# Kernel tuning notes

Hardware: AMD Instinct MI355X
Metric: run time of the kernel (lower is better)

## Reference

```python
import math
import jax, jax.numpy as jnp
import numpy as np

B, N, D, NC, TMAX = 8, 4096, 1024, 512, 1000


def setup_inputs() -> dict:
    key = jax.random.key(0)
    ks = jax.random.split(key, 12)
    tokens = jax.random.normal(ks[0], (B, N, D), jnp.float32)
    ctx_C = jax.random.normal(ks[1], (B, NC, D), jnp.float32)
    t = jax.random.randint(ks[2], (B,), 0, TMAX, dtype=jnp.int32)
    rare_mask = jax.random.bernoulli(ks[3], 0.05, (B, N))
    # Linear params stored as (in, out); scaled so scores straddle 0.5
    ctx_w = jax.random.normal(ks[4], (D, D // 4), jnp.float32) / math.sqrt(D)
    ctx_b = jax.random.normal(ks[5], (D // 4,), jnp.float32) * 0.01
    t_proj_w = jax.random.normal(ks[6], (D, D), jnp.float32) / math.sqrt(D)
    t_proj_b = jax.random.normal(ks[7], (D,), jnp.float32) * 0.01
    HIN = D + D // 4 + D  # 2304
    w1 = jax.random.normal(ks[8], (HIN, D // 2), jnp.float32) / math.sqrt(HIN)
    b1 = jax.random.normal(ks[9], (D // 2,), jnp.float32) * 0.01
    w2 = jax.random.normal(ks[10], (D // 2,), jnp.float32) * 0.1
    b2 = jnp.zeros((1,), jnp.float32)
    return {"tokens": tokens, "ctx_C": ctx_C, "t": t, "rare_mask": rare_mask,
            "ctx_w": ctx_w, "ctx_b": ctx_b, "t_proj_w": t_proj_w,
            "t_proj_b": t_proj_b, "w1": w1, "b1": b1, "w2": w2, "b2": b2}


def reference(tokens, ctx_C, t, rare_mask, ctx_w, ctx_b, t_proj_w, t_proj_b, w1, b1, w2, b2):
    Bb, Nn, Dd = tokens.shape
    half = Dd // 2
    # sinusoidal timestep embedding buffer (matches torch register_buffer)
    freq = jnp.exp(-math.log(10000.0) * jnp.arange(half, dtype=jnp.float32) / max(half - 1, 1))
    # bottlenecked context: mean over ctx tokens -> (B, D//4)
    ctx_bn = ctx_C.mean(axis=1) @ ctx_w + ctx_b
    args = t.astype(jnp.float32)[:, None] * freq[None, :]            # (B, half)
    emb = jnp.concatenate([jnp.sin(args), jnp.cos(args)], axis=-1)   # (B, D)
    t_emb = emb @ t_proj_w + t_proj_b                                # (B, D)
    x = jnp.concatenate([
        tokens,
        jnp.broadcast_to(ctx_bn[:, None, :], (Bb, Nn, Dd // 4)),
        jnp.broadcast_to(t_emb[:, None, :], (Bb, Nn, Dd)),
    ], axis=-1)                                                       # (B, N, 2.25D)
    h = jax.nn.relu(x @ w1 + b1)                                      # (B, N, D//2)
    scores = jax.nn.sigmoid(h @ w2 + b2)                              # (B, N)
    skip = (scores > 0.5) & jnp.logical_not(rare_mask)
    min_active = max(1, int(Nn * 0.2))
    active = jnp.logical_not(skip).sum(axis=-1)                       # (B,)
    deficit = jnp.maximum(min_active - active, 0)                     # (B,)
    masked = jnp.where(skip, scores, jnp.inf)
    rank = jnp.argsort(jnp.argsort(masked, axis=-1), axis=-1)         # rank among skipped, ascending score
    skip = skip & jnp.logical_not(rank < deficit[:, None])
    return skip, scores
```

## Files before the change

### kernel.cpp

```cpp
#include <hip/hip_runtime.h>
#include <math.h>

#define NN 4096
#define DD 1024
#define M_TOT 32768
#define H1 512
#define MIN_ACTIVE 819
#define MARGIN 0.03f
#define MAXFIX 8192

typedef __bf16 bf16x8 __attribute__((ext_vector_type(8)));
typedef float f32x4 __attribute__((ext_vector_type(4)));

__device__ __forceinline__ unsigned short f2bf(float f) {
    unsigned int u = __float_as_uint(f);
    return (unsigned short)((u + 0x7FFFu + ((u >> 16) & 1u)) >> 16);
}

__device__ __forceinline__ void glds16(const unsigned short* g, unsigned short* l) {
    __builtin_amdgcn_global_load_lds(
        (const __attribute__((address_space(1))) unsigned int*)g,
        (__attribute__((address_space(3))) unsigned int*)l, 16, 0, 0);
}

__global__ void convB_kernel(const float* __restrict__ w1, unsigned short* __restrict__ w1tt,
                             const unsigned char* __restrict__ rare, int* __restrict__ mode,
                             int* __restrict__ fixcnt) {
    __shared__ float tile[32][65];
    __shared__ int nonbin, oneoff;
    int t = blockIdx.x;
    int c0 = blockIdx.y * 64;
    int tid = threadIdx.x;
    #pragma unroll
    for (int i = 0; i < 8; ++i) {
        int idx = tid + 256 * i;
        int kk = idx >> 6, cc = idx & 63;
        tile[kk][cc] = w1[(size_t)(t * 32 + kk) * H1 + c0 + cc];
    }
    __syncthreads();
    {
        int cc = tid >> 2, jp = tid & 3;
        int c = c0 + cc;
        int j = jp ^ ((c >> 1) & 3);
        unsigned int w[4];
        #pragma unroll
        for (int q = 0; q < 4; ++q)
            w[q] = (unsigned int)f2bf(tile[j * 8 + 2 * q][cc])
                 | ((unsigned int)f2bf(tile[j * 8 + 2 * q + 1][cc]) << 16);
        uint4 v; v.x = w[0]; v.y = w[1]; v.z = w[2]; v.w = w[3];
        *(uint4*)(w1tt + ((size_t)t * 512 + c) * 32 + jp * 8) = v;
    }
    if (blockIdx.x == 0 && blockIdx.y == 0) {
        if (tid == 0) { nonbin = 0; oneoff = 0; *fixcnt = 0; }
        __syncthreads();
        int lnon = 0, lone = 0;
        for (int i = tid; i < 32768; i += 256) {
            unsigned char b = rare[i];
            if (b > 1) lnon = 1;
            else if (b == 1 && (i & 3) != 0) lone = 1;
        }
        if (lnon) atomicOr(&nonbin, 1);
        if (lone) atomicOr(&oneoff, 1);
        __syncthreads();
        if (tid == 0) *mode = nonbin ? 2 : (oneoff ? 1 : 0);
    }
}

__global__ void pmean_kernel(const float* __restrict__ ctx, float* __restrict__ pmean) {
    int blk = blockIdx.x;
    int b = blk >> 5, dq = (blk >> 3) & 3, nz = blk & 7;
    int d = dq * 256 + threadIdx.x;
    const float* base = ctx + ((size_t)(b * 512 + nz * 64)) * DD + d;
    float acc = 0.f;
    for (int n = 0; n < 64; ++n) acc += base[(size_t)n * DD];
    pmean[(b * 8 + nz) * DD + d] = acc;
}

__global__ void prep_kernel(const float* __restrict__ pmean, const int* __restrict__ t,
                            float* __restrict__ mean, float* __restrict__ embf) {
    int idx = blockIdx.x * 256 + threadIdx.x;
    int b = idx >> 10, j = idx & 1023;
    float s = 0.f;
    for (int nz = 0; nz < 8; ++nz) s += pmean[(b * 8 + nz) * DD + j];
    mean[idx] = s * (1.f / 512.f);
    int jj = j & 511;
    double arg = (double)t[b] * exp((-log(10000.0) / 511.0) * (double)jj);
    embf[idx] = (float)((j < 512) ? sin(arg) : cos(arg));
}

__global__ __launch_bounds__(256) void midk_kernel(
    const float* __restrict__ mean, const float* __restrict__ embf,
    const float* __restrict__ ctx_w, const float* __restrict__ ctx_b,
    const float* __restrict__ tpw, const float* __restrict__ tpb,
    float* __restrict__ ctx_bn, float* __restrict__ t_emb) {
    __shared__ float red8[8][32];
    __shared__ float red4[4][64];
    int tid = threadIdx.x;
    if (blockIdx.x < 64) {
        int b = blockIdx.x >> 3, cg = blockIdx.x & 7;
        int c = cg * 32 + (tid & 31), ks = tid >> 5;
        const float* mb = mean + b * DD + ks * 128;
        const float* wb = ctx_w + (size_t)(ks * 128) * 256 + c;
        float acc = 0.f;
        for (int i = 0; i < 128; ++i) acc += mb[i] * wb[(size_t)i * 256];
        red8[ks][tid & 31] = acc;
        __syncthreads();
        if (tid < 32) {
            float s = 0.f;
            for (int k = 0; k < 8; ++k) s += red8[k][tid];
            ctx_bn[b * 256 + cg * 32 + tid] = s + ctx_b[cg * 32 + tid];
        }
    } else {
        int blk = blockIdx.x - 64;
        int b = blk >> 4, cg = blk & 15;
        int c = cg * 64 + (tid & 63), ks = tid >> 6;
        const float* eb = embf + b * DD + ks * 256;
        const float* wb = tpw + (size_t)(ks * 256) * DD + c;
        float acc = 0.f;
        for (int i = 0; i < 256; ++i) acc += eb[i] * wb[(size_t)i * DD];
        red4[ks][tid & 63] = acc;
        __syncthreads();
        if (tid < 64) {
            float s = red4[0][tid] + red4[1][tid] + red4[2][tid] + red4[3][tid];
            t_emb[b * DD + cg * 64 + tid] = s + tpb[cg * 64 + tid];
        }
    }
}

__global__ void baseh_kernel(const float* __restrict__ ctx_bn, const float* __restrict__ t_emb,
                             const float* __restrict__ w1, const float* __restrict__ b1,
                             float* __restrict__ base_h) {
    __shared__ float red[8][32];
    int b = blockIdx.x, cg = blockIdx.y;
    int c = cg * 32 + (threadIdx.x & 31), ks = threadIdx.x >> 5;
    float acc = 0.f;
    for (int i = 0; i < 160; ++i) {
        int k = ks * 160 + i;
        float v = (k < 256) ? ctx_bn[b * 256 + k] : t_emb[b * DD + k - 256];
        acc += v * w1[(size_t)(1024 + k) * H1 + c];
    }
    red[ks][threadIdx.x & 31] = acc;
    __syncthreads();
    if (threadIdx.x < 32) {
        float s = 0.f;
        for (int k = 0; k < 8; ++k) s += red[k][threadIdx.x];
        base_h[b * H1 + cg * 32 + threadIdx.x] = s + b1[cg * 32 + threadIdx.x];
    }
}

__global__ __launch_bounds__(512, 4) void gemm_kernel(
    const float* __restrict__ tokens, const unsigned short* __restrict__ w1tt,
    const float* __restrict__ baseh, const float* __restrict__ w2,
    float* __restrict__ part) {
    __shared__ unsigned short As[128 * 40];
    __shared__ unsigned short Bs[2][256 * 32];
    __shared__ float red[128][4];
    int tid = threadIdx.x;
    int lane = tid & 63, wid = tid >> 6;
    int wm = wid >> 2, wn = wid & 3;
    int la = lane & 15, lk = lane >> 4;
    int row0 = blockIdx.x * 128;
    int half = blockIdx.y;
    const unsigned short* wsrc = w1tt + (size_t)half * 256 * 32;

    f32x4 acc[4][4];
    #pragma unroll
    for (int i = 0; i < 4; ++i)
        #pragma unroll
        for (int j = 0; j < 4; ++j)
            acc[i][j] = (f32x4){0.f, 0.f, 0.f, 0.f};

    float4 sa[2];
    #define LOAD_A(kt_) { \
        _Pragma("unroll") \
        for (int i = 0; i < 2; ++i) { \
            int id = tid + 512 * i; \
            int r = id >> 3, xk = id & 7; \
            sa[i] = *(const float4*)(tokens + (size_t)(row0 + r) * DD + (kt_) + xk * 4); \
        } }
    #define WRITE_A() { \
        _Pragma("unroll") \
        for (int i = 0; i < 2; ++i) { \
            int id = tid + 512 * i; \
            int r = id >> 3, xk = id & 7; \
            ushort4 h; \
            h.x = f2bf(sa[i].x); h.y = f2bf(sa[i].y); \
            h.z = f2bf(sa[i].z); h.w = f2bf(sa[i].w); \
            *(ushort4*)(As + r * 40 + xk * 4) = h; \
        } }
    #define STAGE_B(t_, bb_) { \
        const unsigned short* gsrc = wsrc + (size_t)(t_) * 512 * 32; \
        _Pragma("unroll") \
        for (int q = 0; q < 2; ++q) { \
            int chunk = wid * 2 + q; \
            glds16(gsrc + chunk * 512 + lane * 8, &Bs[bb_][chunk * 512]); \
        } }

    STAGE_B(0, 0);
    LOAD_A(0);
    WRITE_A();
    __syncthreads();

    for (int t = 0; t < 32; ++t) {
        int bb = t & 1;
        if (t < 31) {
            STAGE_B(t + 1, bb ^ 1);
            LOAD_A((t + 1) * 32);
        }
        bf16x8 af[4], bfr[4];
        #pragma unroll
        for (int mf = 0; mf < 4; ++mf) {
            int r = wm * 64 + mf * 16 + la;
            af[mf] = *(const bf16x8*)(As + r * 40 + lk * 8);
        }
        #pragma unroll
        for (int nf = 0; nf < 4; ++nf) {
            int c = wn * 64 + nf * 16 + la;
            int sw = lk ^ ((c >> 1) & 3);
            bfr[nf] = *(const bf16x8*)(&Bs[bb][c * 32 + sw * 8]);
        }
        #pragma unroll
        for (int mf = 0; mf < 4; ++mf)
            #pragma unroll
            for (int nf = 0; nf < 4; ++nf)
                acc[mf][nf] = __builtin_amdgcn_mfma_f32_16x16x32_bf16(af[mf], bfr[nf], acc[mf][nf], 0, 0, 0);
        __syncthreads();
        if (t < 31) {
            WRITE_A();
            __syncthreads();
        }
    }

    int b = row0 >> 12;
    const float* bh = baseh + b * H1;
    float bhv[4], w2v[4];
    #pragma unroll
    for (int nf = 0; nf < 4; ++nf) {
        int col = half * 256 + wn * 64 + nf * 16 + la;
        bhv[nf] = bh[col];
        w2v[nf] = w2[col];
    }
    #pragma unroll
    for (int mf = 0; mf < 4; ++mf) {
        #pragma unroll
        for (int reg = 0; reg < 4; ++reg) {
            float p = 0.f;
            #pragma unroll
            for (int nf = 0; nf < 4; ++nf) {
                float h = acc[mf][nf][reg] + bhv[nf];
                h = fmaxf(h, 0.f);
                p += h * w2v[nf];
            }
            p += __shfl_xor(p, 1, 64);
            p += __shfl_xor(p, 2, 64);
            p += __shfl_xor(p, 4, 64);
            p += __shfl_xor(p, 8, 64);
            if (la == 0) red[wm * 64 + mf * 16 + lk * 4 + reg][wn] = p;
        }
    }
    __syncthreads();
    if (tid < 128)
        part[(size_t)(row0 + tid) * 2 + half] = red[tid][0] + red[tid][1] + red[tid][2] + red[tid][3];

    #undef LOAD_A
    #undef WRITE_A
    #undef STAGE_B
}

__global__ void score_kernel(const float* __restrict__ part, const float* __restrict__ b2,
                             const void* __restrict__ rare, const int* __restrict__ mode_p,
                             float* __restrict__ out, int* __restrict__ fixcnt,
                             int* __restrict__ fixlist) {
    int row = blockIdx.x * 256 + threadIdx.x;
    float logit = part[(size_t)row * 2] + part[(size_t)row * 2 + 1] + b2[0];
    float score = 1.f / (1.f + expf(-logit));
    int mode = *mode_p;
    bool rm = (mode == 1) ? (((const unsigned char*)rare)[row] != 0)
            : (mode == 2) ? (((const float*)rare)[row] != 0.f)
            : (((const int*)rare)[row] != 0);
    out[row] = ((score > 0.5f) && !rm) ? 1.f : 0.f;
    out[M_TOT + row] = score;
    if (fabsf(logit) < MARGIN) {
        int i = atomicAdd(fixcnt, 1);
        if (i < MAXFIX) fixlist[i] = row;
    }
}

__global__ __launch_bounds__(512) void fixup_kernel(
    const int* __restrict__ fixcnt, const int* __restrict__ fixlist,
    const float* __restrict__ tokens, const float* __restrict__ w1,
    const float* __restrict__ base_h, const float* __restrict__ w2,
    const float* __restrict__ b2, const void* __restrict__ rare,
    const int* __restrict__ mode_p, float* __restrict__ out) {
    __shared__ float tok[DD];
    __shared__ float red[8];
    int tid = threadIdx.x;
    int lane = tid & 63, wid = tid >> 6;
    int n = *fixcnt;
    if (n > MAXFIX) n = MAXFIX;
    for (int g = blockIdx.x; g < n; g += gridDim.x) {
        int row = fixlist[g];
        int b = row >> 12;
        if (tid < 256)
            ((float4*)tok)[tid] = ((const float4*)(tokens + (size_t)row * DD))[tid];
        __syncthreads();
        float acc = 0.f;
        const float* wp = w1 + tid;
        #pragma unroll 8
        for (int k = 0; k < DD; ++k)
            acc += tok[k] * wp[(size_t)k * H1];
        float h = acc + base_h[b * H1 + tid];
        h = fmaxf(h, 0.f);
        float p = h * w2[tid];
        p += __shfl_xor(p, 1, 64);
        p += __shfl_xor(p, 2, 64);
        p += __shfl_xor(p, 4, 64);
        p += __shfl_xor(p, 8, 64);
        p += __shfl_xor(p, 16, 64);
        p += __shfl_xor(p, 32, 64);
        if (lane == 0) red[wid] = p;
        __syncthreads();
        if (tid == 0) {
            float logit = b2[0];
            #pragma unroll
            for (int w = 0; w < 8; ++w) logit += red[w];
            float score = 1.f / (1.f + expf(-logit));
            int mode = *mode_p;
            bool rm = (mode == 1) ? (((const unsigned char*)rare)[row] != 0)
                    : (mode == 2) ? (((const float*)rare)[row] != 0.f)
                    : (((const int*)rare)[row] != 0);
            out[row] = ((score > 0.5f) && !rm) ? 1.f : 0.f;
            out[M_TOT + row] = score;
        }
        __syncthreads();
    }
}

__global__ void floor_kernel(float* __restrict__ out) {
    __shared__ float s[NN];
    __shared__ unsigned char f[NN];
    __shared__ int cnt;
    int b = blockIdx.x, tid = threadIdx.x;
    if (tid == 0) cnt = 0;
    __syncthreads();
    int local = 0;
    for (int i = tid; i < NN; i += 256) {
        s[i] = out[M_TOT + b * NN + i];
        unsigned char sk = out[b * NN + i] > 0.5f;
        f[i] = sk;
        local += sk;
    }
    atomicAdd(&cnt, local);
    __syncthreads();
    int deficit = cnt - (NN - MIN_ACTIVE);
    if (deficit <= 0) return;
    for (int i = tid; i < NN; i += 256) {
        if (!f[i]) continue;
        float si = s[i];
        int rank = 0;
        for (int j = 0; j < NN; ++j) {
            if (f[j] && (s[j] < si || (s[j] == si && j < i))) {
                if (++rank >= deficit) break;
            }
        }
        if (rank < deficit) out[b * NN + i] = 0.f;
    }
}

extern "C" void kernel_launch(void* const* d_in, const int* in_sizes, int n_in,
                              void* d_out, int out_size, void* d_ws, size_t ws_size,
                              hipStream_t stream) {
    const float* tokens   = (const float*)d_in[0];
    const float* ctx_C    = (const float*)d_in[1];
    const int*   t        = (const int*)d_in[2];
    const void*  rare     = d_in[3];
    const float* ctx_w    = (const float*)d_in[4];
    const float* ctx_b    = (const float*)d_in[5];
    const float* t_proj_w = (const float*)d_in[6];
    const float* t_proj_b = (const float*)d_in[7];
    const float* w1       = (const float*)d_in[8];
    const float* b1       = (const float*)d_in[9];
    const float* w2       = (const float*)d_in[10];
    const float* b2       = (const float*)d_in[11];
    float* out = (float*)d_out;

    char* ws = (char*)d_ws;
    unsigned short* w1tt  = (unsigned short*)(ws);
    float* pmean          = (float*)(ws + 1048576);
    float* part           = (float*)(ws + 1048576);
    float* mean           = (float*)(ws + 1310720);
    float* embf           = (float*)(ws + 1343488);
    float* ctx_bn         = (float*)(ws + 1376256);
    float* t_emb          = (float*)(ws + 1384448);
    float* base_h         = (float*)(ws + 1417216);
    int*   mode           = (int*)  (ws + 1433600);
    int*   fixcnt         = (int*)  (ws + 1433664);
    int*   fixlist        = (int*)  (ws + 1433728);

    convB_kernel<<<dim3(32, 8), 256, 0, stream>>>(w1, w1tt, (const unsigned char*)rare, mode, fixcnt);
    pmean_kernel<<<256, 256, 0, stream>>>(ctx_C, pmean);
    prep_kernel<<<32, 256, 0, stream>>>(pmean, t, mean, embf);
    midk_kernel<<<192, 256, 0, stream>>>(mean, embf, ctx_w, ctx_b, t_proj_w, t_proj_b, ctx_bn, t_emb);
    baseh_kernel<<<dim3(8, 16), 256, 0, stream>>>(ctx_bn, t_emb, w1, b1, base_h);
    gemm_kernel<<<dim3(256, 2), 512, 0, stream>>>(tokens, w1tt, base_h, w2, part);
    score_kernel<<<128, 256, 0, stream>>>(part, b2, rare, mode, out, fixcnt, fixlist);
    fixup_kernel<<<512, 512, 0, stream>>>(fixcnt, fixlist, tokens, w1, base_h, w2, b2, rare, mode, out);
    floor_kernel<<<8, 256, 0, stream>>>(out);
}
```

Baseline: 198.2 us.

## Double-buffer A tile in GEMM, fuse convB with pmean, batch fixup rows

The GEMM now double-buffers the A tile in LDS and issues global loads two k-steps ahead. It replaces the two __syncthreads per iteration with one barrier guarded by explicit waitcnt, so the tile conversion and staging overlap the MFMAs. The w1 conversion and ctx partial-mean kernels are merged into one launch to save a kernel launch. The fixup kernel processes four rows per block so each w1 load is reused across rows. The costs are more LDS in the GEMM, which may lower occupancy, and hand-placed waitcnt counts that must stay correct.

```diff
diff --git a/kernel.cpp b/kernel.cpp
--- a/kernel.cpp
+++ b/kernel.cpp
@@ -23,57 +23,59 @@
         (__attribute__((address_space(3))) unsigned int*)l, 16, 0, 0);
 }
 
-__global__ void convB_kernel(const float* __restrict__ w1, unsigned short* __restrict__ w1tt,
-                             const unsigned char* __restrict__ rare, int* __restrict__ mode,
-                             int* __restrict__ fixcnt) {
+__global__ void convB_pmean_kernel(const float* __restrict__ w1, unsigned short* __restrict__ w1tt,
+                                   const float* __restrict__ ctx, float* __restrict__ pmean,
+                                   const unsigned char* __restrict__ rare, int* __restrict__ mode,
+                                   int* __restrict__ fixcnt) {
     __shared__ float tile[32][65];
     __shared__ int nonbin, oneoff;
-    int t = blockIdx.x;
-    int c0 = blockIdx.y * 64;
+    int blk = blockIdx.x;
     int tid = threadIdx.x;
-    #pragma unroll
-    for (int i = 0; i < 8; ++i) {
-        int idx = tid + 256 * i;
-        int kk = idx >> 6, cc = idx & 63;
-        tile[kk][cc] = w1[(size_t)(t * 32 + kk) * H1 + c0 + cc];
-    }
-    __syncthreads();
-    {
-        int cc = tid >> 2, jp = tid & 3;
-        int c = c0 + cc;
-        int j = jp ^ ((c >> 1) & 3);
-        unsigned int w[4];
-        #pragma unroll
-        for (int q = 0; q < 4; ++q)
-            w[q] = (unsigned int)f2bf(tile[j * 8 + 2 * q][cc])
-                 | ((unsigned int)f2bf(tile[j * 8 + 2 * q + 1][cc]) << 16);
-        uint4 v; v.x = w[0]; v.y = w[1]; v.z = w[2]; v.w = w[3];
-        *(uint4*)(w1tt + ((size_t)t * 512 + c) * 32 + jp * 8) = v;
-    }
-    if (blockIdx.x == 0 && blockIdx.y == 0) {
-        if (tid == 0) { nonbin = 0; oneoff = 0; *fixcnt = 0; }
-        __syncthreads();
-        int lnon = 0, lone = 0;
-        for (int i = tid; i < 32768; i += 256) {
-            unsigned char b = rare[i];
-            if (b > 1) lnon = 1;
-            else if (b == 1 && (i & 3) != 0) lone = 1;
-        }
-        if (lnon) atomicOr(&nonbin, 1);
-        if (lone) atomicOr(&oneoff, 1);
-        __syncthreads();
-        if (tid == 0) *mode = nonbin ? 2 : (oneoff ? 1 : 0);
-    }
-}
-
-__global__ void pmean_kernel(const float* __restrict__ ctx, float* __restrict__ pmean) {
-    int blk = blockIdx.x;
-    int b = blk >> 5, dq = (blk >> 3) & 3, nz = blk & 7;
-    int d = dq * 256 + threadIdx.x;
-    const float* base = ctx + ((size_t)(b * 512 + nz * 64)) * DD + d;
-    float acc = 0.f;
-    for (int n = 0; n < 64; ++n) acc += base[(size_t)n * DD];
-    pmean[(b * 8 + nz) * DD + d] = acc;
+    if (blk < 256) {
+        int t = blk >> 3;
+        int c0 = (blk & 7) * 64;
+        #pragma unroll
+        for (int i = 0; i < 8; ++i) {
+            int idx = tid + 256 * i;
+            int kk = idx >> 6, cc = idx & 63;
+            tile[kk][cc] = w1[(size_t)(t * 32 + kk) * H1 + c0 + cc];
+        }
+        __syncthreads();
+        {
+            int cc = tid >> 2, jp = tid & 3;
+            int c = c0 + cc;
+            int j = jp ^ ((c >> 1) & 3);
+            unsigned int w[4];
+            #pragma unroll
+            for (int q = 0; q < 4; ++q)
+                w[q] = (unsigned int)f2bf(tile[j * 8 + 2 * q][cc])
+                     | ((unsigned int)f2bf(tile[j * 8 + 2 * q + 1][cc]) << 16);
+            uint4 v; v.x = w[0]; v.y = w[1]; v.z = w[2]; v.w = w[3];
+            *(uint4*)(w1tt + ((size_t)t * 512 + c) * 32 + jp * 8) = v;
+        }
+        if (blk == 0) {
+            if (tid == 0) { nonbin = 0; oneoff = 0; *fixcnt = 0; }
+            __syncthreads();
+            int lnon = 0, lone = 0;
+            for (int i = tid; i < 32768; i += 256) {
+                unsigned char b = rare[i];
+                if (b > 1) lnon = 1;
+                else if (b == 1 && (i & 3) != 0) lone = 1;
+            }
+            if (lnon) atomicOr(&nonbin, 1);
+            if (lone) atomicOr(&oneoff, 1);
+            __syncthreads();
+            if (tid == 0) *mode = nonbin ? 2 : (oneoff ? 1 : 0);
+        }
+    } else {
+        int pblk = blk - 256;
+        int b = pblk >> 5, dq = (pblk >> 3) & 3, nz = pblk & 7;
+        int d = dq * 256 + tid;
+        const float* base = ctx + ((size_t)(b * 512 + nz * 64)) * DD + d;
+        float acc = 0.f;
+        for (int n = 0; n < 64; ++n) acc += base[(size_t)n * DD];
+        pmean[(b * 8 + nz) * DD + d] = acc;
+    }
 }
 
 __global__ void prep_kernel(const float* __restrict__ pmean, const int* __restrict__ t,
@@ -152,7 +154,7 @@
     const float* __restrict__ tokens, const unsigned short* __restrict__ w1tt,
     const float* __restrict__ baseh, const float* __restrict__ w2,
     float* __restrict__ part) {
-    __shared__ unsigned short As[128 * 40];
+    __shared__ unsigned short As[2][128 * 40];
     __shared__ unsigned short Bs[2][256 * 32];
     __shared__ float red[128][4];
     int tid = threadIdx.x;
@@ -178,7 +180,7 @@
             int r = id >> 3, xk = id & 7; \
             sa[i] = *(const float4*)(tokens + (size_t)(row0 + r) * DD + (kt_) + xk * 4); \
         } }
-    #define WRITE_A() { \
+    #define WRITE_A(bb_) { \
         _Pragma("unroll") \
         for (int i = 0; i < 2; ++i) { \
             int id = tid + 512 * i; \
@@ -186,7 +188,7 @@
             ushort4 h; \
             h.x = f2bf(sa[i].x); h.y = f2bf(sa[i].y); \
             h.z = f2bf(sa[i].z); h.w = f2bf(sa[i].w); \
-            *(ushort4*)(As + r * 40 + xk * 4) = h; \
+            *(ushort4*)(&As[bb_][r * 40 + xk * 4]) = h; \
         } }
     #define STAGE_B(t_, bb_) { \
         const unsigned short* gsrc = wsrc + (size_t)(t_) * 512 * 32; \
@@ -198,20 +200,19 @@
 
     STAGE_B(0, 0);
     LOAD_A(0);
-    WRITE_A();
-    __syncthreads();
+    WRITE_A(0);
+    LOAD_A(32);
+    asm volatile("s_waitcnt lgkmcnt(0)" ::: "memory");
+    __builtin_amdgcn_s_barrier();
+    __builtin_amdgcn_sched_barrier(0);
 
     for (int t = 0; t < 32; ++t) {
         int bb = t & 1;
-        if (t < 31) {
-            STAGE_B(t + 1, bb ^ 1);
-            LOAD_A((t + 1) * 32);
-        }
         bf16x8 af[4], bfr[4];
         #pragma unroll
         for (int mf = 0; mf < 4; ++mf) {
             int r = wm * 64 + mf * 16 + la;
-            af[mf] = *(const bf16x8*)(As + r * 40 + lk * 8);
+            af[mf] = *(const bf16x8*)(&As[bb][r * 40 + lk * 8]);
         }
         #pragma unroll
         for (int nf = 0; nf < 4; ++nf) {
@@ -219,17 +220,28 @@
             int sw = lk ^ ((c >> 1) & 3);
             bfr[nf] = *(const bf16x8*)(&Bs[bb][c * 32 + sw * 8]);
         }
+        if (t < 31) {
+            WRITE_A(bb ^ 1);
+            STAGE_B(t + 1, bb ^ 1);
+            __builtin_amdgcn_sched_barrier(0);
+            if (t < 30) LOAD_A((t + 2) * 32);
+        }
         #pragma unroll
         for (int mf = 0; mf < 4; ++mf)
             #pragma unroll
             for (int nf = 0; nf < 4; ++nf)
                 acc[mf][nf] = __builtin_amdgcn_mfma_f32_16x16x32_bf16(af[mf], bfr[nf], acc[mf][nf], 0, 0, 0);
-        __syncthreads();
         if (t < 31) {
-            WRITE_A();
-            __syncthreads();
-        }
-    }
+            if (t < 30) asm volatile("s_waitcnt vmcnt(2)" ::: "memory");
+            else        asm volatile("s_waitcnt vmcnt(0)" ::: "memory");
+            asm volatile("s_waitcnt lgkmcnt(0)" ::: "memory");
+            __builtin_amdgcn_s_barrier();
+            __builtin_amdgcn_sched_barrier(0);
+        }
+    }
+    #undef LOAD_A
+    #undef WRITE_A
+    #undef STAGE_B
 
     int b = row0 >> 12;
     const float* bh = baseh + b * H1;
@@ -261,10 +273,6 @@
     __syncthreads();
     if (tid < 128)
         part[(size_t)(row0 + tid) * 2 + half] = red[tid][0] + red[tid][1] + red[tid][2] + red[tid][3];
-
-    #undef LOAD_A
-    #undef WRITE_A
-    #undef STAGE_B
 }
 
 __global__ void score_kernel(const float* __restrict__ part, const float* __restrict__ b2,
@@ -292,38 +300,54 @@
     const float* __restrict__ base_h, const float* __restrict__ w2,
     const float* __restrict__ b2, const void* __restrict__ rare,
     const int* __restrict__ mode_p, float* __restrict__ out) {
-    __shared__ float tok[DD];
-    __shared__ float red[8];
+    __shared__ float tok[4][DD];
+    __shared__ float redm[4][8];
+    __shared__ int rows_s[4];
     int tid = threadIdx.x;
     int lane = tid & 63, wid = tid >> 6;
     int n = *fixcnt;
     if (n > MAXFIX) n = MAXFIX;
-    for (int g = blockIdx.x; g < n; g += gridDim.x) {
-        int row = fixlist[g];
-        int b = row >> 12;
-        if (tid < 256)
-            ((float4*)tok)[tid] = ((const float4*)(tokens + (size_t)row * DD))[tid];
-        __syncthreads();
-        float acc = 0.f;
+    int ng = (n + 3) >> 2;
+    for (int g = blockIdx.x; g < ng; g += gridDim.x) {
+        int base = g * 4;
+        int nr = n - base; if (nr > 4) nr = 4;
+        if (tid < 4) rows_s[tid] = fixlist[base + (tid < nr ? tid : 0)];
+        __syncthreads();
+        for (int i = tid; i < nr * 256; i += 512) {
+            int r = i >> 8, off = i & 255;
+            ((float4*)tok[r])[off] =
+                ((const float4*)(tokens + (size_t)rows_s[r] * DD))[off];
+        }
+        __syncthreads();
+        float a0 = 0.f, a1 = 0.f, a2 = 0.f, a3 = 0.f;
         const float* wp = w1 + tid;
-        #pragma unroll 8
-        for (int k = 0; k < DD; ++k)
-            acc += tok[k] * wp[(size_t)k * H1];
-        float h = acc + base_h[b * H1 + tid];
-        h = fmaxf(h, 0.f);
-        float p = h * w2[tid];
-        p += __shfl_xor(p, 1, 64);
-        p += __shfl_xor(p, 2, 64);
-        p += __shfl_xor(p, 4, 64);
-        p += __shfl_xor(p, 8, 64);
-        p += __shfl_xor(p, 16, 64);
-        p += __shfl_xor(p, 32, 64);
-        if (lane == 0) red[wid] = p;
-        __syncthreads();
-        if (tid == 0) {
+        #pragma unroll 4
+        for (int k = 0; k < DD; ++k) {
+            float w = wp[(size_t)k * H1];
+            a0 += tok[0][k] * w; a1 += tok[1][k] * w;
+            a2 += tok[2][k] * w; a3 += tok[3][k] * w;
+        }
+        float av[4] = {a0, a1, a2, a3};
+        #pragma unroll
+        for (int r = 0; r < 4; ++r) {
+            int brow = rows_s[r] >> 12;
+            float h = av[r] + base_h[brow * H1 + tid];
+            h = fmaxf(h, 0.f);
+            float p = h * w2[tid];
+            p += __shfl_xor(p, 1, 64);
+            p += __shfl_xor(p, 2, 64);
+            p += __shfl_xor(p, 4, 64);
+            p += __shfl_xor(p, 8, 64);
+            p += __shfl_xor(p, 16, 64);
+            p += __shfl_xor(p, 32, 64);
+            if (lane == 0) redm[r][wid] = p;
+        }
+        __syncthreads();
+        if (tid < nr) {
+            int row = rows_s[tid];
             float logit = b2[0];
             #pragma unroll
-            for (int w = 0; w < 8; ++w) logit += red[w];
+            for (int w = 0; w < 8; ++w) logit += redm[tid][w];
             float score = 1.f / (1.f + expf(-logit));
             int mode = *mode_p;
             bool rm = (mode == 1) ? (((const unsigned char*)rare)[row] != 0)
@@ -397,13 +421,13 @@
     int*   fixcnt         = (int*)  (ws + 1433664);
     int*   fixlist        = (int*)  (ws + 1433728);
 
-    convB_kernel<<<dim3(32, 8), 256, 0, stream>>>(w1, w1tt, (const unsigned char*)rare, mode, fixcnt);
-    pmean_kernel<<<256, 256, 0, stream>>>(ctx_C, pmean);
+    convB_pmean_kernel<<<512, 256, 0, stream>>>(w1, w1tt, ctx_C, pmean,
+                                                (const unsigned char*)rare, mode, fixcnt);
     prep_kernel<<<32, 256, 0, stream>>>(pmean, t, mean, embf);
     midk_kernel<<<192, 256, 0, stream>>>(mean, embf, ctx_w, ctx_b, t_proj_w, t_proj_b, ctx_bn, t_emb);
     baseh_kernel<<<dim3(8, 16), 256, 0, stream>>>(ctx_bn, t_emb, w1, b1, base_h);
     gemm_kernel<<<dim3(256, 2), 512, 0, stream>>>(tokens, w1tt, base_h, w2, part);
     score_kernel<<<128, 256, 0, stream>>>(part, b2, rare, mode, out, fixcnt, fixlist);
-    fixup_kernel<<<512, 512, 0, stream>>>(fixcnt, fixlist, tokens, w1, base_h, w2, b2, rare, mode, out);
+    fixup_kernel<<<256, 512, 0, stream>>>(fixcnt, fixlist, tokens, w1, base_h, w2, b2, rare, mode, out);
     floor_kernel<<<8, 256, 0, stream>>>(out);
 }
```

New measurement: 194.1 us. 1.02x faster.
